# Kernel optimization log

Hardware: AMD Instinct MI355X
Metric: run time of the kernel (lower is better)

## Reference

```python
import jax, jax.numpy as jnp
import numpy as np

B, S, D, H = 4, 2048, 1024, 16
HD = D // H  # head size = 64


def setup_inputs() -> dict:
    key = jax.random.key(0)
    ks = jax.random.split(key, 9)
    scale = 1.0 / np.sqrt(D)
    x = jax.random.normal(ks[0], (B, S, D), dtype=jnp.float32)
    Wq = jax.random.normal(ks[1], (D, D), dtype=jnp.float32) * scale
    Wk = jax.random.normal(ks[2], (D, D), dtype=jnp.float32) * scale
    Wv = jax.random.normal(ks[3], (D, D), dtype=jnp.float32) * scale
    Wo = jax.random.normal(ks[4], (D, D), dtype=jnp.float32) * scale
    bq = jax.random.normal(ks[5], (D,), dtype=jnp.float32) * 0.01
    bk = jax.random.normal(ks[6], (D,), dtype=jnp.float32) * 0.01
    bv = jax.random.normal(ks[7], (D,), dtype=jnp.float32) * 0.01
    bo = jax.random.normal(ks[8], (D,), dtype=jnp.float32) * 0.01
    return {"x": x, "Wq": Wq, "bq": bq, "Wk": Wk, "bk": bk,
            "Wv": Wv, "bv": bv, "Wo": Wo, "bo": bo}


def reference(x, Wq, bq, Wk, bk, Wv, bv, Wo, bo):
    Bv, Sv, Dv = x.shape
    # QKV projections (torch Linear: x @ W^T + b; here W stored as [in, out])
    q = x @ Wq + bq  # [B,S,D]
    k = x @ Wk + bk
    v = x @ Wv + bv
    # split heads -> [B,H,S,HD]
    q = q.reshape(Bv, Sv, H, HD).transpose(0, 2, 1, 3)
    k = k.reshape(Bv, Sv, H, HD).transpose(0, 2, 1, 3)
    v = v.reshape(Bv, Sv, H, HD).transpose(0, 2, 1, 3)
    # scaled scores + additive causal mask (upper triangle -> -inf)
    scores = jnp.einsum('bhqd,bhkd->bhqk', q, k) * (1.0 / np.sqrt(HD))
    causal = jnp.triu(jnp.full((Sv, Sv), -jnp.inf, dtype=scores.dtype), k=1)
    attn = jax.nn.softmax(scores + causal, axis=-1)
    # dropout is identity in eval / p=0
    out = jnp.einsum('bhqk,bhkd->bhqd', attn, v)
    out = out.transpose(0, 2, 1, 3).reshape(Bv, Sv, Dv)
    return out @ Wo + bo
```

## Files before the change

### kernel.cpp

```cpp
#include <hip/hip_runtime.h>
#include <hip/hip_bf16.h>


typedef unsigned short u16;
typedef short bf16x8 __attribute__((ext_vector_type(8)));
typedef float f32x4 __attribute__((ext_vector_type(4)));

constexpr int NB = 4, NS = 2048, ND = 1024, NH = 16, NHD = 64;
constexpr int NM = NB * NS;
constexpr float NEG = -1e30f;
constexpr int EPAD = 136;
constexpr float KEXP = 0.125f * 1.4426950408889634f;

#if __has_builtin(__builtin_amdgcn_exp2f)
#define EXP2(x) __builtin_amdgcn_exp2f(x)
#else
#define EXP2(x) exp2f(x)
#endif

__device__ __forceinline__ u16 f2bf(float f) {
  union { float f; unsigned int u; } c; c.f = f;
  unsigned int r = (c.u + 0x7FFFu + ((c.u >> 16) & 1u)) >> 16;
  return (u16)r;
}
__device__ __forceinline__ unsigned int pk2bf(float a, float b) {
  float2 t; t.x = a; t.y = b;
  __hip_bfloat162 h = __float22bfloat162_rn(t);
  unsigned int u; __builtin_memcpy(&u, &h, 4); return u;
}
__device__ __forceinline__ void g2lds16(const u16* g, u16* l) {
  __builtin_amdgcn_global_load_lds(
      (const __attribute__((address_space(1))) void*)g,
      (__attribute__((address_space(3))) void*)l, 16, 0, 0);
}
__device__ __forceinline__ bf16x8 ldsw(const u16* b, int row, int cq) {
  return *(const bf16x8*)&b[row * 64 + ((cq ^ (row & 7)) << 3)];
}

__global__ __launch_bounds__(256) void fill_kernel(float* __restrict__ p, float v, int n) {
  int i = blockIdx.x * 256 + threadIdx.x;
  if (i < n) p[i] = v;
}

__global__ __launch_bounds__(256) void cvt_kernel(const float* __restrict__ in,
                                                  u16* __restrict__ out, int n4) {
  int i = blockIdx.x * 256 + threadIdx.x;
  if (i < n4) {
    float4 f = ((const float4*)in)[i];
    ushort4 o;
    o.x = f2bf(f.x); o.y = f2bf(f.y); o.z = f2bf(f.z); o.w = f2bf(f.w);
    ((ushort4*)out)[i] = o;
  }
}

__global__ __launch_bounds__(256) void wt_kernel(
    const float* __restrict__ s0, const float* __restrict__ s1,
    const float* __restrict__ s2, const float* __restrict__ s3,
    u16* __restrict__ d0, u16* __restrict__ d1,
    u16* __restrict__ d2, u16* __restrict__ d3) {
  const int z = blockIdx.z;
  const float* S = (z == 0) ? s0 : (z == 1) ? s1 : (z == 2) ? s2 : s3;
  u16* D = (z == 0) ? d0 : (z == 1) ? d1 : (z == 2) ? d2 : d3;
  const float sc = (z == 0) ? KEXP : 1.0f;
  __shared__ u16 t[64][68];
  const int r0 = blockIdx.x * 64, c0 = blockIdx.y * 64;
  const int tid = threadIdx.x;
#pragma unroll
  for (int i = 0; i < 4; i++) {
    int row = (tid >> 4) + i * 16;
    int col = (tid & 15) * 4;
    float4 f = *(const float4*)&S[(long)(r0 + row) * ND + c0 + col];
    ushort4 u;
    u.x = f2bf(f.x * sc); u.y = f2bf(f.y * sc);
    u.z = f2bf(f.z * sc); u.w = f2bf(f.w * sc);
    *(ushort4*)&t[row][col] = u;
  }
  __syncthreads();
#pragma unroll
  for (int i = 0; i < 4; i++) {
    int nrow = (tid >> 4) + i * 16;
    int kcol = (tid & 15) * 4;
    ushort4 u;
    u.x = t[kcol + 0][nrow]; u.y = t[kcol + 1][nrow];
    u.z = t[kcol + 2][nrow]; u.w = t[kcol + 3][nrow];
    *(ushort4*)&D[(long)(c0 + nrow) * ND + r0 + kcol] = u;
  }
}

__global__ __launch_bounds__(256, 3) void gemm_qkv_kernel(
    const float* __restrict__ Xf, const u16* __restrict__ Xb,
    const u16* __restrict__ WtQ,
    const float* __restrict__ bqp, const float* __restrict__ bkp,
    const float* __restrict__ bvp,
    u16* __restrict__ Qw, u16* __restrict__ Kw, u16* __restrict__ Vtw,
    int xmode) {
  __shared__ __attribute__((aligned(16))) u16 SMEM[128 * EPAD];
  u16* Asm = SMEM;
  u16* Bsm = SMEM + 8192;
  const int m0 = blockIdx.x * 128;
  const int ng = blockIdx.y;
  const int mat = ng >> 3, n0 = (ng & 7) * 128;
  const u16* Wt = WtQ + (long)mat * ND * ND;
  const int tid = threadIdx.x;
  const int w = tid >> 6, lane = tid & 63, quad = lane >> 4, lr = lane & 15;
  const int wm = w & 1, wn = w >> 1;
  const int b_r = lane >> 3, b_c = lane & 7;

  f32x4 acc[4][4] = {};

  for (int k0 = 0; k0 < ND; k0 += 64) {
    __syncthreads();
    if (xmode == 0) {
#pragma unroll
      for (int j = 0; j < 4; j++) {
        int r = w * 32 + j * 8 + b_r;
        const float* src = Xf + (long)(m0 + r) * ND + k0 + ((b_c ^ (r & 7)) << 3);
        float4 f0 = *(const float4*)src;
        float4 f1 = *(const float4*)(src + 4);
        uint4 d;
        d.x = pk2bf(f0.x, f0.y); d.y = pk2bf(f0.z, f0.w);
        d.z = pk2bf(f1.x, f1.y); d.w = pk2bf(f1.z, f1.w);
        *(uint4*)&Asm[r * 64 + (b_c << 3)] = d;
      }
    } else {
#pragma unroll
      for (int j = 0; j < 4; j++) {
        int R0 = w * 32 + j * 8;
        int r = R0 + b_r;
        g2lds16(Xb + (long)(m0 + r) * ND + k0 + ((b_c ^ (r & 7)) << 3),
                &Asm[R0 * 64]);
      }
    }
#pragma unroll
    for (int j = 0; j < 4; j++) {
      int R0 = w * 32 + j * 8;
      int r = R0 + b_r;
      g2lds16(Wt + (long)(n0 + r) * ND + k0 + ((b_c ^ (r & 7)) << 3),
              &Bsm[R0 * 64]);
    }
    __syncthreads();

#pragma unroll
    for (int kk = 0; kk < 2; kk++) {
      bf16x8 af[4], bfr[4];
#pragma unroll
      for (int mt = 0; mt < 4; mt++)
        af[mt] = ldsw(Asm, wm * 64 + mt * 16 + lr, kk * 4 + quad);
#pragma unroll
      for (int nt = 0; nt < 4; nt++)
        bfr[nt] = ldsw(Bsm, wn * 64 + nt * 16 + lr, kk * 4 + quad);
#pragma unroll
      for (int nt = 0; nt < 4; nt++)
#pragma unroll
        for (int mt = 0; mt < 4; mt++)
          acc[nt][mt] = __builtin_amdgcn_mfma_f32_16x16x32_bf16(
              af[mt], bfr[nt], acc[nt][mt], 0, 0, 0);
    }
  }

  const float* bias = (mat == 0) ? bqp : (mat == 1) ? bkp : bvp;
  const float bsc = (mat == 0) ? KEXP : 1.0f;
  __syncthreads();
  if (mat < 2) {
#pragma unroll
    for (int nt = 0; nt < 4; nt++) {
      int n_loc = wn * 64 + nt * 16 + lr;
      float bn = bias[n0 + n_loc] * bsc;
#pragma unroll
      for (int mt = 0; mt < 4; mt++)
#pragma unroll
        for (int r = 0; r < 4; r++) {
          int m_loc = wm * 64 + mt * 16 + quad * 4 + r;
          SMEM[m_loc * EPAD + n_loc] = f2bf(acc[nt][mt][r] + bn);
        }
    }
    __syncthreads();
    u16* Yv = (mat == 0) ? Qw : Kw;
#pragma unroll
    for (int pass = 0; pass < 8; pass++) {
      int row = pass * 16 + (tid >> 4), c = tid & 15;
      uint4 d = *(const uint4*)&SMEM[row * EPAD + c * 8];
      int n_g = n0 + c * 8, h_ = n_g >> 6, hd_ = n_g & (NHD - 1);
      int m = m0 + row, b_ = m >> 11, s_ = m & (NS - 1);
      *(uint4*)&Yv[((long)((b_ * NH + h_) * NS + s_)) * NHD + hd_] = d;
    }
  } else {
#pragma unroll
    for (int nt = 0; nt < 4; nt++) {
      int n_loc = wn * 64 + nt * 16 + lr;
      float bn = bias[n0 + n_loc];
#pragma unroll
      for (int mt = 0; mt < 4; mt++) {
        int m_base = wm * 64 + mt * 16 + quad * 4;
        uint2 d;
        d.x = pk2bf(acc[nt][mt][0] + bn, acc[nt][mt][1] + bn);
        d.y = pk2bf(acc[nt][mt][2] + bn, acc[nt][mt][3] + bn);
        *(uint2*)&SMEM[n_loc * EPAD + m_base] = d;
      }
    }
    __syncthreads();
#pragma unroll
    for (int pass = 0; pass < 8; pass++) {
      int plane = pass * 16 + (tid >> 4), mc = tid & 15;
      uint4 d = *(const uint4*)&SMEM[plane * EPAD + mc * 8];
      int n_g = n0 + plane, h_ = n_g >> 6, hd_ = n_g & (NHD - 1);
      int m = m0 + mc * 8, b_ = m >> 11, s_ = m & (NS - 1);
      long base = ((long)((b_ * NH + h_) * NHD + hd_)) * NS;
      int cb = s_ & ~31;
      int s1 = (mc & 1) * 16 + ((mc >> 1) & 1) * 4;
      uint2 lo; lo.x = d.x; lo.y = d.y;
      uint2 hi; hi.x = d.z; hi.y = d.w;
      *(uint2*)&Vtw[base + cb + s1] = lo;
      *(uint2*)&Vtw[base + cb + s1 + 8] = hi;
    }
  }
}

__global__ __launch_bounds__(256, 3) void gemm_out_kernel(
    const u16* __restrict__ Xg, const u16* __restrict__ Wt,
    const float* __restrict__ bias, float* __restrict__ Y) {
  __shared__ __attribute__((aligned(16))) u16 Asm[128 * 64];
  __shared__ __attribute__((aligned(16))) u16 Bsm[128 * 64];
  const int m0 = blockIdx.x * 128, n0 = blockIdx.y * 128;
  const int tid = threadIdx.x;
  const int w = tid >> 6, lane = tid & 63, quad = lane >> 4, lr = lane & 15;
  const int wm = w & 1, wn = w >> 1;
  const int b_r = lane >> 3, b_c = lane & 7;

  f32x4 acc[4][4] = {};

  for (int k0 = 0; k0 < ND; k0 += 64) {
    __syncthreads();
    const int h_ = k0 >> 6;
#pragma unroll
    for (int j = 0; j < 4; j++) {
      int R0 = w * 32 + j * 8;
      int r = R0 + b_r;
      int mrow = m0 + r, b_ = mrow >> 11, s_ = mrow & (NS - 1);
      g2lds16(Xg + ((long)((b_ * NH + h_) * NS + s_)) * NHD + ((b_c ^ (r & 7)) << 3),
              &Asm[R0 * 64]);
      g2lds16(Wt + (long)(n0 + r) * ND + k0 + ((b_c ^ (r & 7)) << 3),
              &Bsm[R0 * 64]);
    }
    __syncthreads();

#pragma unroll
    for (int kk = 0; kk < 2; kk++) {
      bf16x8 af[4], bfr[4];
#pragma unroll
      for (int mt = 0; mt < 4; mt++)
        af[mt] = ldsw(Asm, wm * 64 + mt * 16 + lr, kk * 4 + quad);
#pragma unroll
      for (int nt = 0; nt < 4; nt++)
        bfr[nt] = ldsw(Bsm, wn * 64 + nt * 16 + lr, kk * 4 + quad);
#pragma unroll
      for (int nt = 0; nt < 4; nt++)
#pragma unroll
        for (int mt = 0; mt < 4; mt++)
          acc[nt][mt] = __builtin_amdgcn_mfma_f32_16x16x32_bf16(
              af[mt], bfr[nt], acc[nt][mt], 0, 0, 0);
    }
  }

#pragma unroll
  for (int nt = 0; nt < 4; nt++) {
    int n = n0 + wn * 64 + nt * 16 + lr;
    float bn = bias[n];
#pragma unroll
    for (int mt = 0; mt < 4; mt++) {
#pragma unroll
      for (int r = 0; r < 4; r++) {
        int m = m0 + wm * 64 + mt * 16 + quad * 4 + r;
        Y[(long)m * ND + n] = acc[nt][mt][r] + bn;
      }
    }
  }
}

__global__ __launch_bounds__(512) void attn_kernel(
    u16* __restrict__ Q, const u16* __restrict__ K, const u16* __restrict__ Vtg) {
  __shared__ __attribute__((aligned(16))) u16 Klds[2][64 * 64];
  __shared__ __attribute__((aligned(16))) u16 Vt[2][64 * 64];
  const int bh = blockIdx.x;
  const int qt = 15 - blockIdx.y;
  const int q0 = qt * 128;
  const int tid = threadIdx.x;
  const int w = tid >> 6, lane = tid & 63, quad = lane >> 4, lr = lane & 15;
  u16* Qb = Q + (long)bh * NS * NHD;
  const u16* Kb = K + (long)bh * NS * NHD;
  const u16* Vb = Vtg + (long)bh * NHD * NS;

  const int qw0 = q0 + w * 16;
  bf16x8 qf[2];
  {
    int m = qw0 + lr;
    qf[0] = *(const bf16x8*)&Qb[(long)m * NHD + quad * 8];
    qf[1] = *(const bf16x8*)&Qb[(long)m * NHD + 32 + quad * 8];
  }
  const bf16x8 ones = {0x3F80, 0x3F80, 0x3F80, 0x3F80,
                       0x3F80, 0x3F80, 0x3F80, 0x3F80};

  f32x4 oaccT[4] = {};
  f32x4 lacc = {};

  const int sr = lane >> 3;
  const int ssw = (((lane & 7) ^ sr) << 3);
  const int krow0 = w * 8;
  const int ntile = q0 / 64 + 2;

  g2lds16(Kb + (long)(krow0 + sr) * NHD + ssw, &Klds[0][krow0 * 64]);
  g2lds16(Vb + (long)(krow0 + sr) * NS + 0 + ssw, &Vt[0][krow0 * 64]);

  for (int ti = 0; ti < ntile; ti++) {
    const int j0 = ti * 64;
    const int cur = ti & 1;
    if (ti + 1 < ntile) {
      const int j1 = j0 + 64;
      g2lds16(Kb + (long)(j1 + krow0 + sr) * NHD + ssw, &Klds[cur ^ 1][krow0 * 64]);
      g2lds16(Vb + (long)(krow0 + sr) * NS + j1 + ssw, &Vt[cur ^ 1][krow0 * 64]);
      asm volatile("s_waitcnt vmcnt(2)" ::: "memory");
    } else {
      asm volatile("s_waitcnt vmcnt(0)" ::: "memory");
    }
    __builtin_amdgcn_s_barrier();
    __builtin_amdgcn_sched_barrier(0);

    if (j0 <= qw0 + 15) {
      f32x4 scT[4] = {};
#pragma unroll
      for (int t = 0; t < 4; t++) {
        int kr = t * 16 + lr;
        bf16x8 kf0 = ldsw(Klds[cur], kr, quad);
        bf16x8 kf1 = ldsw(Klds[cur], kr, 4 + quad);
        scT[t] = __builtin_amdgcn_mfma_f32_16x16x32_bf16(kf0, qf[0], scT[t], 0, 0, 0);
        scT[t] = __builtin_amdgcn_mfma_f32_16x16x32_bf16(kf1, qf[1], scT[t], 0, 0, 0);
      }

      if (j0 + 63 > qw0) {
#pragma unroll
        for (int t = 0; t < 4; t++)
#pragma unroll
          for (int r = 0; r < 4; r++)
            if ((j0 + t * 16 + quad * 4 + r) > (qw0 + lr)) scT[t][r] = NEG;
      }

#pragma unroll
      for (int t = 0; t < 4; t++)
#pragma unroll
        for (int r = 0; r < 4; r++) scT[t][r] = EXP2(scT[t][r]);

#pragma unroll
      for (int kk = 0; kk < 2; kk++) {
        uint4 pu;
        pu.x = pk2bf(scT[2 * kk][0], scT[2 * kk][1]);
        pu.y = pk2bf(scT[2 * kk][2], scT[2 * kk][3]);
        pu.z = pk2bf(scT[2 * kk + 1][0], scT[2 * kk + 1][1]);
        pu.w = pk2bf(scT[2 * kk + 1][2], scT[2 * kk + 1][3]);
        bf16x8 pt; __builtin_memcpy(&pt, &pu, 16);
        lacc = __builtin_amdgcn_mfma_f32_16x16x32_bf16(ones, pt, lacc, 0, 0, 0);
#pragma unroll
        for (int dt = 0; dt < 4; dt++) {
          bf16x8 va = ldsw(Vt[cur], dt * 16 + lr, kk * 4 + quad);
          oaccT[dt] = __builtin_amdgcn_mfma_f32_16x16x32_bf16(va, pt, oaccT[dt], 0, 0, 0);
        }
      }
    }
    __builtin_amdgcn_s_barrier();
  }

  const float inv = 1.0f / lacc[0];
#pragma unroll
  for (int dt = 0; dt < 4; dt++) {
    uint2 o;
    o.x = pk2bf(oaccT[dt][0] * inv, oaccT[dt][1] * inv);
    o.y = pk2bf(oaccT[dt][2] * inv, oaccT[dt][3] * inv);
    *(uint2*)&Qb[(long)(qw0 + lr) * NHD + dt * 16 + quad * 4] = o;
  }
}

extern "C" void kernel_launch(void* const* d_in, const int* in_sizes, int n_in,
                              void* d_out, int out_size, void* d_ws, size_t ws_size,
                              hipStream_t stream) {
  const float* x  = (const float*)d_in[0];
  const float* Wq = (const float*)d_in[1];
  const float* bq = (const float*)d_in[2];
  const float* Wk = (const float*)d_in[3];
  const float* bk = (const float*)d_in[4];
  const float* Wv = (const float*)d_in[5];
  const float* bv = (const float*)d_in[6];
  const float* Wo = (const float*)d_in[7];
  const float* bo = (const float*)d_in[8];

  const size_t BUF = (size_t)NM * ND * sizeof(u16);
  if (ws_size < 2 * BUF) {
    fill_kernel<<<(out_size + 255) / 256, 256, 0, stream>>>((float*)d_out, 0.f, out_size);
    return;
  }

  u16* Qw  = (u16*)d_ws;
  u16* Vtw = Qw + (long)NM * ND;
  u16* Kw  = (u16*)d_out;
  u16* WtQ = Kw + (long)NM * ND;
  u16* WtO = WtQ + 3L * ND * ND;
  const bool bigws = ws_size >= 3 * BUF;
  u16* Xb = bigws ? (Vtw + (long)NM * ND) : nullptr;

  wt_kernel<<<dim3(16, 16, 4), 256, 0, stream>>>(Wq, Wk, Wv, Wo,
      WtQ, WtQ + (long)ND * ND, WtQ + 2L * ND * ND, WtO);
  if (bigws)
    cvt_kernel<<<(NM * ND / 4 + 255) / 256, 256, 0, stream>>>(x, Xb, NM * ND / 4);

  gemm_qkv_kernel<<<dim3(64, 24), 256, 0, stream>>>(
      x, Xb, WtQ, bq, bk, bv, Qw, Kw, Vtw, bigws ? 2 : 0);
  attn_kernel<<<dim3(NB * NH, NS / 128), 512, 0, stream>>>(Qw, Kw, Vtw);
  hipMemcpyAsync(Vtw, WtO, (size_t)ND * ND * sizeof(u16),
                 hipMemcpyDeviceToDevice, stream);
  gemm_out_kernel<<<dim3(64, 8), 256, 0, stream>>>(Qw, Vtw, bo, (float*)d_out);
}
```

Before: 234.7 us.

## Fuse weight/x prep kernels, enlarge attention tile to 256 queries, skip WtO copy

Merges the weight-transpose and x-to-bf16 conversion into one prep kernel launch with an extra z-slice. The attention kernel now uses 1024-thread blocks covering 256 query rows, with half the waves loading K and half loading V, so each K/V tile in LDS serves twice as many queries. When the workspace is large enough, the transposed output weight goes to a spare buffer so the device-to-device memcpy is skipped. The risks are lower occupancy and fewer attention blocks (512), plus more causal-mask imbalance per block.

```diff
diff --git a/kernel.cpp b/kernel.cpp
--- a/kernel.cpp
+++ b/kernel.cpp
@@ -42,29 +42,31 @@
   if (i < n) p[i] = v;
 }
 
-__global__ __launch_bounds__(256) void cvt_kernel(const float* __restrict__ in,
-                                                  u16* __restrict__ out, int n4) {
-  int i = blockIdx.x * 256 + threadIdx.x;
-  if (i < n4) {
-    float4 f = ((const float4*)in)[i];
-    ushort4 o;
-    o.x = f2bf(f.x); o.y = f2bf(f.y); o.z = f2bf(f.z); o.w = f2bf(f.w);
-    ((ushort4*)out)[i] = o;
-  }
-}
-
-__global__ __launch_bounds__(256) void wt_kernel(
+__global__ __launch_bounds__(256) void prep_kernel(
     const float* __restrict__ s0, const float* __restrict__ s1,
     const float* __restrict__ s2, const float* __restrict__ s3,
     u16* __restrict__ d0, u16* __restrict__ d1,
-    u16* __restrict__ d2, u16* __restrict__ d3) {
+    u16* __restrict__ d2, u16* __restrict__ d3,
+    const float* __restrict__ xin, u16* __restrict__ xout) {
   const int z = blockIdx.z;
+  const int tid = threadIdx.x;
+  if (z == 4) {
+    if (!xout) return;
+    const int n4 = NM * ND / 4;
+    int base = (blockIdx.y * 16 + blockIdx.x) * 256 + tid;
+    for (int i = base; i < n4; i += 65536) {
+      float4 f = ((const float4*)xin)[i];
+      ushort4 o;
+      o.x = f2bf(f.x); o.y = f2bf(f.y); o.z = f2bf(f.z); o.w = f2bf(f.w);
+      ((ushort4*)xout)[i] = o;
+    }
+    return;
+  }
   const float* S = (z == 0) ? s0 : (z == 1) ? s1 : (z == 2) ? s2 : s3;
   u16* D = (z == 0) ? d0 : (z == 1) ? d1 : (z == 2) ? d2 : d3;
   const float sc = (z == 0) ? KEXP : 1.0f;
   __shared__ u16 t[64][68];
   const int r0 = blockIdx.x * 64, c0 = blockIdx.y * 64;
-  const int tid = threadIdx.x;
 #pragma unroll
   for (int i = 0; i < 4; i++) {
     int row = (tid >> 4) + i * 16;
@@ -277,13 +279,13 @@
   }
 }
 
-__global__ __launch_bounds__(512) void attn_kernel(
+__global__ __launch_bounds__(1024) void attn_kernel(
     u16* __restrict__ Q, const u16* __restrict__ K, const u16* __restrict__ Vtg) {
   __shared__ __attribute__((aligned(16))) u16 Klds[2][64 * 64];
   __shared__ __attribute__((aligned(16))) u16 Vt[2][64 * 64];
   const int bh = blockIdx.x;
-  const int qt = 15 - blockIdx.y;
-  const int q0 = qt * 128;
+  const int qt = 7 - blockIdx.y;
+  const int q0 = qt * 256;
   const int tid = threadIdx.x;
   const int w = tid >> 6, lane = tid & 63, quad = lane >> 4, lr = lane & 15;
   u16* Qb = Q + (long)bh * NS * NHD;
@@ -305,20 +307,23 @@
 
   const int sr = lane >> 3;
   const int ssw = (((lane & 7) ^ sr) << 3);
-  const int krow0 = w * 8;
-  const int ntile = q0 / 64 + 2;
-
-  g2lds16(Kb + (long)(krow0 + sr) * NHD + ssw, &Klds[0][krow0 * 64]);
-  g2lds16(Vb + (long)(krow0 + sr) * NS + 0 + ssw, &Vt[0][krow0 * 64]);
+  const int krow0 = (w & 7) * 8;
+  const bool isK = w < 8;
+  const int ntile = q0 / 64 + 4;
+
+  if (isK) g2lds16(Kb + (long)(krow0 + sr) * NHD + ssw, &Klds[0][krow0 * 64]);
+  else     g2lds16(Vb + (long)(krow0 + sr) * NS + 0 + ssw, &Vt[0][krow0 * 64]);
 
   for (int ti = 0; ti < ntile; ti++) {
     const int j0 = ti * 64;
     const int cur = ti & 1;
     if (ti + 1 < ntile) {
       const int j1 = j0 + 64;
-      g2lds16(Kb + (long)(j1 + krow0 + sr) * NHD + ssw, &Klds[cur ^ 1][krow0 * 64]);
-      g2lds16(Vb + (long)(krow0 + sr) * NS + j1 + ssw, &Vt[cur ^ 1][krow0 * 64]);
-      asm volatile("s_waitcnt vmcnt(2)" ::: "memory");
+      if (isK)
+        g2lds16(Kb + (long)(j1 + krow0 + sr) * NHD + ssw, &Klds[cur ^ 1][krow0 * 64]);
+      else
+        g2lds16(Vb + (long)(krow0 + sr) * NS + j1 + ssw, &Vt[cur ^ 1][krow0 * 64]);
+      asm volatile("s_waitcnt vmcnt(1)" ::: "memory");
     } else {
       asm volatile("s_waitcnt vmcnt(0)" ::: "memory");
     }
@@ -392,6 +397,7 @@
   const float* bo = (const float*)d_in[8];
 
   const size_t BUF = (size_t)NM * ND * sizeof(u16);
+  const size_t WSZ = (size_t)ND * ND * sizeof(u16);
   if (ws_size < 2 * BUF) {
     fill_kernel<<<(out_size + 255) / 256, 256, 0, stream>>>((float*)d_out, 0.f, out_size);
     return;
@@ -404,16 +410,22 @@
   u16* WtO = WtQ + 3L * ND * ND;
   const bool bigws = ws_size >= 3 * BUF;
   u16* Xb = bigws ? (Vtw + (long)NM * ND) : nullptr;
-
-  wt_kernel<<<dim3(16, 16, 4), 256, 0, stream>>>(Wq, Wk, Wv, Wo,
-      WtQ, WtQ + (long)ND * ND, WtQ + 2L * ND * ND, WtO);
-  if (bigws)
-    cvt_kernel<<<(NM * ND / 4 + 255) / 256, 256, 0, stream>>>(x, Xb, NM * ND / 4);
+  u16* spare = (ws_size >= 3 * BUF + WSZ) ? (Xb + (long)NM * ND) : nullptr;
+  u16* wto_dst = spare ? spare : WtO;
+
+  prep_kernel<<<dim3(16, 16, 5), 256, 0, stream>>>(
+      Wq, Wk, Wv, Wo,
+      WtQ, WtQ + (long)ND * ND, WtQ + 2L * ND * ND, wto_dst, x, Xb);
 
   gemm_qkv_kernel<<<dim3(64, 24), 256, 0, stream>>>(
       x, Xb, WtQ, bq, bk, bv, Qw, Kw, Vtw, bigws ? 2 : 0);
-  attn_kernel<<<dim3(NB * NH, NS / 128), 512, 0, stream>>>(Qw, Kw, Vtw);
-  hipMemcpyAsync(Vtw, WtO, (size_t)ND * ND * sizeof(u16),
-                 hipMemcpyDeviceToDevice, stream);
-  gemm_out_kernel<<<dim3(64, 8), 256, 0, stream>>>(Qw, Vtw, bo, (float*)d_out);
-}
+  attn_kernel<<<dim3(NB * NH, NS / 256), 1024, 0, stream>>>(Qw, Kw, Vtw);
+  u16* wto_src;
+  if (spare) {
+    wto_src = spare;
+  } else {
+    hipMemcpyAsync(Vtw, WtO, WSZ, hipMemcpyDeviceToDevice, stream);
+    wto_src = Vtw;
+  }
+  gemm_out_kernel<<<dim3(64, 8), 256, 0, stream>>>(Qw, wto_src, bo, (float*)d_out);
+}
```

Result: slower. 245.0 us (+4.4%).
